# Performance work log

Hardware: AMD Instinct MI355X
Metric: run time of the kernel (lower is better)

## Reference

```python
import jax, jax.numpy as jnp
import numpy as np
import math

D_MODEL = 1024
NUM_HEADS = 16
D_KV = 64
INNER = NUM_HEADS * D_KV
NUM_BUCKETS = 32
MAX_DISTANCE = 128


def _relative_position_bucket(relative_position, num_buckets=NUM_BUCKETS, max_distance=MAX_DISTANCE):
    # bidirectional T5 bucketing
    n = -relative_position
    num_buckets = num_buckets // 2
    ret = (n < 0).astype(jnp.int32) * num_buckets
    n = jnp.abs(n)
    max_exact = num_buckets // 2
    is_small = n < max_exact
    n_safe = jnp.maximum(n, 1).astype(jnp.float32)  # avoid log(0); masked by is_small
    val_if_large = max_exact + (
        jnp.log(n_safe / max_exact) / math.log(max_distance / max_exact) * (num_buckets - max_exact)
    ).astype(jnp.int32)
    val_if_large = jnp.minimum(val_if_large, num_buckets - 1)
    return jnp.where(is_small, n, val_if_large) + ret


def _position_bias(rel_emb, q_len, k_len):
    ctx = jnp.arange(q_len)[:, None]
    mem = jnp.arange(k_len)[None, :]
    buckets = _relative_position_bucket(mem - ctx)          # [q, k]
    values = rel_emb[buckets]                               # [q, k, H]
    return jnp.transpose(values, (2, 0, 1))[None]           # [1, H, q, k]


def setup_inputs() -> dict:
    key = jax.random.key(0)
    ks = jax.random.split(key, 6)
    B, S = 2, 2048
    scale = 1.0 / math.sqrt(D_MODEL)
    return {
        "hidden_states": jax.random.normal(ks[0], (B, S, D_MODEL), dtype=jnp.float32),
        "mask": jnp.zeros((B, 1, 1, S), dtype=jnp.float32),
        "Wq": jax.random.normal(ks[1], (D_MODEL, INNER), dtype=jnp.float32) * scale,
        "Wk": jax.random.normal(ks[2], (D_MODEL, INNER), dtype=jnp.float32) * scale,
        "Wv": jax.random.normal(ks[3], (D_MODEL, INNER), dtype=jnp.float32) * scale,
        "Wo": jax.random.normal(ks[4], (INNER, D_MODEL), dtype=jnp.float32) * scale,
        "rel_emb": jax.random.normal(ks[5], (NUM_BUCKETS, NUM_HEADS), dtype=jnp.float32),
    }


def reference(hidden_states, mask, Wq, Wk, Wv, Wo, rel_emb):
    B, S, _ = hidden_states.shape
    def split_heads(x):
        return jnp.transpose(x.reshape(B, -1, NUM_HEADS, D_KV), (0, 2, 1, 3))  # [B,H,S,d]
    q = split_heads(hidden_states @ Wq)
    k = split_heads(hidden_states @ Wk)
    v = split_heads(hidden_states @ Wv)
    scores = jnp.einsum("bhqd,bhkd->bhqk", q, k)            # unscaled, T5-style
    position_bias = _position_bias(rel_emb, S, S)           # [1,H,S,S]
    scores = scores + position_bias + mask
    attn = jax.nn.softmax(scores, axis=-1)
    context = jnp.einsum("bhqk,bhkd->bhqd", attn, v)
    context = jnp.transpose(context, (0, 2, 1, 3)).reshape(B, S, INNER)
    output = context @ Wo
    return output, position_bias
```

## Files before the change

kernel.cpp:

```cpp
#include <hip/hip_runtime.h>
#include <cstdint>

#define AS1 __attribute__((address_space(1)))
#define AS3 __attribute__((address_space(3)))

typedef _Float16 half8 __attribute__((ext_vector_type(8)));
typedef _Float16 half4_t __attribute__((ext_vector_type(4)));
typedef float v4f __attribute__((ext_vector_type(4)));

__device__ __forceinline__ void async_ld16(const void* g, void* l) {
  __builtin_amdgcn_global_load_lds((const AS1 uint32_t*)g, (AS3 uint32_t*)l, 16, 0, 0);
}

__device__ __forceinline__ int t5_bucket(int delta) {
  int n = -delta;
  int ret = 0;
  if (n < 0) { ret = 16; n = -n; }
  if (n < 8) return n + ret;
  if (n >= 91) return 15 + ret;
  if ((n & (n - 1)) == 0) {
    int l = 31 - __clz(n);
    int v = 2 + 2 * l;
    return (v > 15 ? 15 : v) + ret;
  }
  int v = 8 + (int)(logf((float)n * 0.125f) * (8.0f / logf(16.0f)));
  return (v > 15 ? 15 : v) + ret;
}

__global__ void k_prep(const float* __restrict__ hs, const float* __restrict__ Wq,
                       const float* __restrict__ Wk, const float* __restrict__ Wv,
                       const float* __restrict__ Wo, _Float16* __restrict__ hsF,
                       _Float16* __restrict__ wqkvT, _Float16* __restrict__ woT) {
  const int tid = threadIdx.x;
  if (blockIdx.x < 4096) {
    int t = blockIdx.x * 256 + tid;
    float4 f = ((const float4*)hs)[t];
    half4_t h = {(_Float16)f.x, (_Float16)f.y, (_Float16)f.z, (_Float16)f.w};
    ((half4_t*)hsF)[t] = h;
    return;
  }
  __shared__ float tile[32][33];
  const int idx = blockIdx.x - 4096;
  const int z = idx >> 10, rem = idx & 1023;
  const float* src = (z == 0) ? Wq : (z == 1) ? Wk : (z == 2) ? Wv : Wo;
  _Float16* dst = (z < 3) ? (wqkvT + ((size_t)z << 20)) : woT;
  const int tx = tid & 31, ty = tid >> 5;
  const int bx = (rem & 31) * 32, by = (rem >> 5) * 32;
#pragma unroll
  for (int i = 0; i < 32; i += 8)
    tile[ty + i][tx] = src[(size_t)(by + ty + i) * 1024 + bx + tx];
  __syncthreads();
#pragma unroll
  for (int i = 0; i < 32; i += 8)
    dst[(size_t)(bx + ty + i) * 1024 + by + tx] = (_Float16)tile[tx][ty + i];
}

__global__ __launch_bounds__(256, 2) void k_gemm_qkv_bias(
    const _Float16* __restrict__ A, const _Float16* __restrict__ BT,
    _Float16* __restrict__ qkv, _Float16* __restrict__ vT,
    const float* __restrict__ rel, float* __restrict__ outb) {
  __shared__ __align__(16) _Float16 As[128 * 32];
  __shared__ __align__(16) _Float16 Bs[128 * 32];
  __shared__ float btab[256];
  const int tid = threadIdx.x;
  const int wave = tid >> 6, lane = tid & 63;
  const int l15 = lane & 15, quad = lane >> 4;
  const int m0 = blockIdx.y * 128, n0 = blockIdx.x * 128;
  const int wm = (wave >> 1) * 64, wn = (wave & 1) * 64;
  const int r0 = tid >> 2, c0 = (tid & 3) * 8;
  constexpr int K = 1024;

  const int bid = blockIdx.y * 24 + blockIdx.x;
  const bool do_bias = bid < 512;
  const int hB = bid >> 5;
  const int qoff = (bid & 31) * 64;
  float c_past = 0.f, c_fut = 0.f;
  if (do_bias) {
    btab[tid & 255] = rel[t5_bucket((tid & 255) - 128) * 16 + hB];
    c_past = rel[15 * 16 + hB];
    c_fut = rel[31 * 16 + hB];
  }

  v4f acc[4][4] = {};
  for (int k0 = 0; k0 < K; k0 += 32) {
    __syncthreads();
    async_ld16(A + (size_t)(m0 + r0) * K + k0 + c0, (char*)As + (size_t)(wave * 64) * 16);
    async_ld16(A + (size_t)(m0 + 64 + r0) * K + k0 + c0,
               (char*)As + (size_t)(256 + wave * 64) * 16);
    async_ld16(BT + (size_t)(n0 + r0) * K + k0 + c0, (char*)Bs + (size_t)(wave * 64) * 16);
    async_ld16(BT + (size_t)(n0 + 64 + r0) * K + k0 + c0,
               (char*)Bs + (size_t)(256 + wave * 64) * 16);
    __syncthreads();

    if (do_bias) {
      const int iter = k0 >> 5;
#pragma unroll
      for (int j = 0; j < 4; ++j) {
        int fi = iter * 1024 + j * 256 + tid;
        int qr = qoff + (fi >> 9);
        int kb = (fi & 511) * 4;
        float4 v;
        if (kb - qr >= 91) {
          v = make_float4(c_fut, c_fut, c_fut, c_fut);
        } else if (qr - kb - 3 >= 91) {
          v = make_float4(c_past, c_past, c_past, c_past);
        } else {
          v.x = btab[kb + 0 - qr + 128];
          v.y = btab[kb + 1 - qr + 128];
          v.z = btab[kb + 2 - qr + 128];
          v.w = btab[kb + 3 - qr + 128];
        }
        ((float4*)outb)[(size_t)bid * 32768 + fi] = v;
      }
    }

    half8 af[4], bf[4];
#pragma unroll
    for (int mt = 0; mt < 4; ++mt)
      af[mt] = *(const half8*)(As + (wm + mt * 16 + l15) * 32 + quad * 8);
#pragma unroll
    for (int nt = 0; nt < 4; ++nt)
      bf[nt] = *(const half8*)(Bs + (wn + nt * 16 + l15) * 32 + quad * 8);
#pragma unroll
    for (int mt = 0; mt < 4; ++mt)
#pragma unroll
      for (int nt = 0; nt < 4; ++nt)
        acc[mt][nt] = __builtin_amdgcn_mfma_f32_16x16x32_f16(af[mt], bf[nt], acc[mt][nt], 0, 0, 0);
  }
  if (n0 >= 2048) {
#pragma unroll
    for (int mt = 0; mt < 4; ++mt)
#pragma unroll
      for (int nt = 0; nt < 4; ++nt) {
        int col = n0 + wn + nt * 16 + l15 - 2048;
        int row0 = m0 + wm + mt * 16 + quad * 4;
        int bb = row0 >> 11, s0 = row0 & 2047;
        half4_t hv = {(_Float16)acc[mt][nt][0], (_Float16)acc[mt][nt][1],
                      (_Float16)acc[mt][nt][2], (_Float16)acc[mt][nt][3]};
        *(half4_t*)(vT + ((size_t)bb * 1024 + col) * 2048 + s0) = hv;
      }
    return;
  }
#pragma unroll
  for (int mt = 0; mt < 4; ++mt)
#pragma unroll
    for (int nt = 0; nt < 4; ++nt)
#pragma unroll
      for (int r = 0; r < 4; ++r)
        qkv[(size_t)(m0 + wm + mt * 16 + quad * 4 + r) * 3072 + n0 + wn + nt * 16 + l15] =
            (_Float16)acc[mt][nt][r];
}

__global__ __launch_bounds__(256, 2) void k_gemm_n64(const _Float16* __restrict__ A,
                                                     const _Float16* __restrict__ BT,
                                                     float* __restrict__ C, int K, int ldc) {
  __shared__ __align__(16) _Float16 As[128 * 32];
  __shared__ __align__(16) _Float16 Bs[64 * 32];
  const int tid = threadIdx.x;
  const int wave = tid >> 6, lane = tid & 63;
  const int l15 = lane & 15, quad = lane >> 4;
  const int m0 = blockIdx.y * 128, n0 = blockIdx.x * 64;
  const int wm = (wave >> 1) * 64, wn = (wave & 1) * 32;
  const int r0 = tid >> 2, c0 = (tid & 3) * 8;
  v4f acc[4][2] = {};
  for (int k0 = 0; k0 < K; k0 += 32) {
    __syncthreads();
    async_ld16(A + (size_t)(m0 + r0) * K + k0 + c0, (char*)As + (size_t)(wave * 64) * 16);
    async_ld16(A + (size_t)(m0 + 64 + r0) * K + k0 + c0,
               (char*)As + (size_t)(256 + wave * 64) * 16);
    async_ld16(BT + (size_t)(n0 + r0) * K + k0 + c0, (char*)Bs + (size_t)(wave * 64) * 16);
    __syncthreads();
    half8 af[4], bf[2];
#pragma unroll
    for (int mt = 0; mt < 4; ++mt)
      af[mt] = *(const half8*)(As + (wm + mt * 16 + l15) * 32 + quad * 8);
#pragma unroll
    for (int nt = 0; nt < 2; ++nt)
      bf[nt] = *(const half8*)(Bs + (wn + nt * 16 + l15) * 32 + quad * 8);
#pragma unroll
    for (int mt = 0; mt < 4; ++mt)
#pragma unroll
      for (int nt = 0; nt < 2; ++nt)
        acc[mt][nt] = __builtin_amdgcn_mfma_f32_16x16x32_f16(af[mt], bf[nt], acc[mt][nt], 0, 0, 0);
  }
#pragma unroll
  for (int mt = 0; mt < 4; ++mt)
#pragma unroll
    for (int nt = 0; nt < 2; ++nt)
#pragma unroll
      for (int r = 0; r < 4; ++r)
        C[(size_t)(m0 + wm + mt * 16 + quad * 4 + r) * ldc + n0 + wn + nt * 16 + l15] =
            acc[mt][nt][r];
}

__global__ __launch_bounds__(256, 2) void k_attn(const _Float16* __restrict__ qkv,
                                                 const _Float16* __restrict__ vT,
                                                 const float* __restrict__ mask,
                                                 const float* __restrict__ rel,
                                                 _Float16* __restrict__ ctx) {
  constexpr int S = 2048, LD = 3072;
  __shared__ __align__(16) _Float16 Ks[2][64 * 72];
  __shared__ __align__(16) _Float16 VT[2][64 * 72];
  __shared__ __align__(16) _Float16 Psh[128 * 72];
  __shared__ float btab[512];
  const int tid = threadIdx.x, wave = tid >> 6, lane = tid & 63;
  const int l15 = lane & 15, quad = lane >> 4;
  const int q0 = blockIdx.x * 128, h = blockIdx.y, b = blockIdx.z;

  for (int j = tid; j < 512; j += 256) btab[j] = rel[t5_bucket(j - 256) * 16 + h];
  const float c_past = rel[15 * 16 + h];
  const float c_fut = rel[31 * 16 + h];

  half8 bq[2][2];
#pragma unroll
  for (int qt = 0; qt < 2; ++qt) {
    const _Float16* qp = qkv + (size_t)(b * S + q0 + wave * 32 + qt * 16 + l15) * LD + h * 64;
    bq[qt][0] = *(const half8*)(qp + quad * 8);
    bq[qt][1] = *(const half8*)(qp + 32 + quad * 8);
  }
  v4f o[2][4] = {};
  float mrun[2] = {-INFINITY, -INFINITY};
  float lrun[2] = {0.f, 0.f};

  const int srow = tid >> 2, scol = (tid & 3) * 8;
  const _Float16* kg = qkv + (size_t)(b * S + srow) * LD + 1024 + h * 64 + scol;
  const _Float16* vg = vT + ((size_t)((b * 16 + h) * 64 + srow)) * S + scol;
  const float4* mkp = (const float4*)(mask + (size_t)b * S);

  {
    half8 kr0 = *(const half8*)(kg);
    half8 kr1 = *(const half8*)(kg + 32);
    half8 vr0 = *(const half8*)(vg);
    half8 vr1 = *(const half8*)(vg + 32);
    *(half8*)(&Ks[0][srow * 72 + scol]) = kr0;
    *(half8*)(&Ks[0][srow * 72 + scol + 32]) = kr1;
    *(half8*)(&VT[0][srow * 72 + scol]) = vr0;
    *(half8*)(&VT[0][srow * 72 + scol + 32]) = vr1;
  }
  float4 mk[4];
#pragma unroll
  for (int mt = 0; mt < 4; ++mt) mk[mt] = mkp[mt * 4 + quad];
  __syncthreads();

  for (int kv0 = 0; kv0 < S; kv0 += 64) {
    const int buf = (kv0 >> 6) & 1;
    const bool more = (kv0 + 64) < S;
    half8 kr0n, kr1n, vr0n, vr1n;
    float4 mkn[4];
    if (more) {
      kr0n = *(const half8*)(kg + (size_t)(kv0 + 64) * LD);
      kr1n = *(const half8*)(kg + (size_t)(kv0 + 64) * LD + 32);
      vr0n = *(const half8*)(vg + kv0 + 64);
      vr1n = *(const half8*)(vg + kv0 + 64 + 32);
#pragma unroll
      for (int mt = 0; mt < 4; ++mt) mkn[mt] = mkp[((kv0 + 64) >> 2) + mt * 4 + quad];
    }

    const _Float16* KsB = &Ks[buf][0];
    const _Float16* VTB = &VT[buf][0];
    v4f sc[2][4] = {};
#pragma unroll
    for (int kc = 0; kc < 2; ++kc)
#pragma unroll
      for (int mt = 0; mt < 4; ++mt) {
        half8 af = *(const half8*)(KsB + (mt * 16 + l15) * 72 + kc * 32 + quad * 8);
        sc[0][mt] = __builtin_amdgcn_mfma_f32_16x16x32_f16(af, bq[0][kc], sc[0][mt], 0, 0, 0);
        sc[1][mt] = __builtin_amdgcn_mfma_f32_16x16x32_f16(af, bq[1][kc], sc[1][mt], 0, 0, 0);
      }

    const int diff = kv0 - q0;
    const bool mixed = (diff >= -153) && (diff <= 217);
    const float cf = (diff >= 218) ? c_fut : c_past;
    v4f cm[4];
#pragma unroll
    for (int mt = 0; mt < 4; ++mt) {
      cm[mt][0] = mk[mt].x; cm[mt][1] = mk[mt].y; cm[mt][2] = mk[mt].z; cm[mt][3] = mk[mt].w;
      if (!mixed) {
        cm[mt][0] += cf; cm[mt][1] += cf; cm[mt][2] += cf; cm[mt][3] += cf;
      }
    }
    if (mixed) {
#pragma unroll
      for (int qt = 0; qt < 2; ++qt) {
        const int qq = q0 + wave * 32 + qt * 16 + l15;
#pragma unroll
        for (int mt = 0; mt < 4; ++mt) {
          int base = kv0 + mt * 16 + quad * 4 - qq + 256;
#pragma unroll
          for (int r = 0; r < 4; ++r) sc[qt][mt][r] += btab[base + r] + cm[mt][r];
        }
      }
    } else {
#pragma unroll
      for (int qt = 0; qt < 2; ++qt)
#pragma unroll
        for (int mt = 0; mt < 4; ++mt)
#pragma unroll
          for (int r = 0; r < 4; ++r) sc[qt][mt][r] += cm[mt][r];
    }

#pragma unroll
    for (int qt = 0; qt < 2; ++qt) {
      v4f m4 = sc[qt][0];
#pragma unroll
      for (int r = 0; r < 4; ++r) {
        m4[r] = fmaxf(m4[r], sc[qt][1][r]);
        m4[r] = fmaxf(m4[r], sc[qt][2][r]);
        m4[r] = fmaxf(m4[r], sc[qt][3][r]);
      }
      float mx = fmaxf(fmaxf(m4[0], m4[1]), fmaxf(m4[2], m4[3]));
      mx = fmaxf(mx, __shfl_xor(mx, 16, 64));
      mx = fmaxf(mx, __shfl_xor(mx, 32, 64));
      float mnew = fmaxf(mrun[qt], mx);
      float alpha = __expf(mrun[qt] - mnew);
      mrun[qt] = mnew;
      v4f s4 = {};
#pragma unroll
      for (int mt = 0; mt < 4; ++mt)
#pragma unroll
        for (int r = 0; r < 4; ++r) {
          float p = __expf(sc[qt][mt][r] - mnew);
          sc[qt][mt][r] = p;
          s4[r] += p;
        }
      float rs = (s4[0] + s4[1]) + (s4[2] + s4[3]);
      rs += __shfl_xor(rs, 16, 64);
      rs += __shfl_xor(rs, 32, 64);
      lrun[qt] = lrun[qt] * alpha + rs;
#pragma unroll
      for (int dt = 0; dt < 4; ++dt)
#pragma unroll
        for (int r = 0; r < 4; ++r) o[qt][dt][r] *= alpha;
      const int prow = wave * 32 + qt * 16 + l15;
#pragma unroll
      for (int mt = 0; mt < 4; ++mt) {
        half4_t ph = {(_Float16)sc[qt][mt][0], (_Float16)sc[qt][mt][1],
                      (_Float16)sc[qt][mt][2], (_Float16)sc[qt][mt][3]};
        *(half4_t*)(Psh + prow * 72 + mt * 16 + quad * 4) = ph;
      }
    }

#pragma unroll
    for (int kc = 0; kc < 2; ++kc) {
      half8 bp0 = *(const half8*)(Psh + (wave * 32 + l15) * 72 + kc * 32 + quad * 8);
      half8 bp1 = *(const half8*)(Psh + (wave * 32 + 16 + l15) * 72 + kc * 32 + quad * 8);
#pragma unroll
      for (int dt = 0; dt < 4; ++dt) {
        half8 av = *(const half8*)(VTB + (dt * 16 + l15) * 72 + kc * 32 + quad * 8);
        o[0][dt] = __builtin_amdgcn_mfma_f32_16x16x32_f16(av, bp0, o[0][dt], 0, 0, 0);
        o[1][dt] = __builtin_amdgcn_mfma_f32_16x16x32_f16(av, bp1, o[1][dt], 0, 0, 0);
      }
    }

    if (more) {
      _Float16* Kn = &Ks[buf ^ 1][0];
      _Float16* Vn = &VT[buf ^ 1][0];
      *(half8*)(Kn + srow * 72 + scol) = kr0n;
      *(half8*)(Kn + srow * 72 + scol + 32) = kr1n;
      *(half8*)(Vn + srow * 72 + scol) = vr0n;
      *(half8*)(Vn + srow * 72 + scol + 32) = vr1n;
      __syncthreads();
#pragma unroll
      for (int mt = 0; mt < 4; ++mt) mk[mt] = mkn[mt];
    }
  }
#pragma unroll
  for (int qt = 0; qt < 2; ++qt) {
    float inv = 1.0f / lrun[qt];
    const size_t token = (size_t)(b * S + q0 + wave * 32 + qt * 16 + l15);
#pragma unroll
    for (int dt = 0; dt < 4; ++dt) {
      half4_t hv = {(_Float16)(o[qt][dt][0] * inv), (_Float16)(o[qt][dt][1] * inv),
                    (_Float16)(o[qt][dt][2] * inv), (_Float16)(o[qt][dt][3] * inv)};
      *(half4_t*)(ctx + token * 1024 + h * 64 + dt * 16 + quad * 4) = hv;
    }
  }
}

extern "C" void kernel_launch(void* const* d_in, const int* in_sizes, int n_in,
                              void* d_out, int out_size, void* d_ws, size_t ws_size,
                              hipStream_t stream) {
  const float* hs = (const float*)d_in[0];
  const float* mask = (const float*)d_in[1];
  const float* Wq = (const float*)d_in[2];
  const float* Wk = (const float*)d_in[3];
  const float* Wv = (const float*)d_in[4];
  const float* Wo = (const float*)d_in[5];
  const float* rel = (const float*)d_in[6];
  float* out = (float*)d_out;

  char* ws = (char*)d_ws;
  _Float16* hsF = (_Float16*)(ws);
  _Float16* wqkvT = (_Float16*)(ws + (8u << 20));
  _Float16* woT = (_Float16*)(ws + (14u << 20));
  _Float16* qkv = (_Float16*)(ws + (16u << 20));
  _Float16* ctx = (_Float16*)(ws + (40u << 20));
  _Float16* vT = (_Float16*)(ws + (48u << 20));

  k_prep<<<8192, 256, 0, stream>>>(hs, Wq, Wk, Wv, Wo, hsF, wqkvT, woT);

  k_gemm_qkv_bias<<<dim3(24, 32), 256, 0, stream>>>(hsF, wqkvT, qkv, vT, rel,
                                                    out + 4194304);
  k_attn<<<dim3(16, 16, 2), 256, 0, stream>>>(qkv, vT, mask, rel, ctx);
  k_gemm_n64<<<dim3(16, 32), 256, 0, stream>>>(ctx, woT, out, 1024, 1024);
}
```

Baseline: 427.4 us.

## Split position-bias output writes between QKV GEMM and attention kernels; skip redundant rescale

```diff
diff --git a/kernel.cpp b/kernel.cpp
--- a/kernel.cpp
+++ b/kernel.cpp
@@ -95,10 +95,12 @@
     if (do_bias) {
       const int iter = k0 >> 5;
 #pragma unroll
-      for (int j = 0; j < 4; ++j) {
-        int fi = iter * 1024 + j * 256 + tid;
-        int qr = qoff + (fi >> 9);
-        int kb = (fi & 511) * 4;
+      for (int j = 0; j < 2; ++j) {
+        int fi = iter * 512 + j * 256 + tid;
+        int qr = qoff + (fi >> 8);
+        int c = fi & 255;
+        int k4 = ((c >> 4) << 5) + (c & 15);
+        int kb = k4 << 2;
         float4 v;
         if (kb - qr >= 91) {
           v = make_float4(c_fut, c_fut, c_fut, c_fut);
@@ -110,7 +112,7 @@
           v.z = btab[kb + 2 - qr + 128];
           v.w = btab[kb + 3 - qr + 128];
         }
-        ((float4*)outb)[(size_t)bid * 32768 + fi] = v;
+        ((float4*)outb)[((size_t)hB * 2048 + qr) * 512 + k4] = v;
       }
     }
 
@@ -197,7 +199,8 @@
                                                  const _Float16* __restrict__ vT,
                                                  const float* __restrict__ mask,
                                                  const float* __restrict__ rel,
-                                                 _Float16* __restrict__ ctx) {
+                                                 _Float16* __restrict__ ctx,
+                                                 float* __restrict__ outb) {
   constexpr int S = 2048, LD = 3072;
   __shared__ __align__(16) _Float16 Ks[2][64 * 72];
   __shared__ __align__(16) _Float16 VT[2][64 * 72];
@@ -226,6 +229,9 @@
   const _Float16* kg = qkv + (size_t)(b * S + srow) * LD + 1024 + h * 64 + scol;
   const _Float16* vg = vT + ((size_t)((b * 16 + h) * 64 + srow)) * S + scol;
   const float4* mkp = (const float4*)(mask + (size_t)b * S);
+
+  const int qrow0 = q0 + b * 64;
+  float4* const bias_base = (float4*)outb + ((size_t)h * 2048 + qrow0) * 512;
 
   {
     half8 kr0 = *(const half8*)(kg);
@@ -256,6 +262,46 @@
       for (int mt = 0; mt < 4; ++mt) mkn[mt] = mkp[((kv0 + 64) >> 2) + mt * 4 + quad];
     }
 
+    if (kv0 & 64) {
+      const int diffw = kv0 - qrow0;
+      float4* dst = bias_base + (kv0 >> 2);
+      if (diffw >= 154) {
+        const float4 v = make_float4(c_fut, c_fut, c_fut, c_fut);
+#pragma unroll
+        for (int j = 0; j < 4; ++j) {
+          int fi = j * 256 + tid;
+          dst[(size_t)(fi >> 4) * 512 + (fi & 15)] = v;
+        }
+      } else if (diffw <= -154) {
+        const float4 v = make_float4(c_past, c_past, c_past, c_past);
+#pragma unroll
+        for (int j = 0; j < 4; ++j) {
+          int fi = j * 256 + tid;
+          dst[(size_t)(fi >> 4) * 512 + (fi & 15)] = v;
+        }
+      } else {
+#pragma unroll
+        for (int j = 0; j < 4; ++j) {
+          int fi = j * 256 + tid;
+          int row = fi >> 4, c4 = fi & 15;
+          int q = qrow0 + row, k = kv0 + c4 * 4;
+          float4 v;
+          if (k - q >= 91) {
+            v = make_float4(c_fut, c_fut, c_fut, c_fut);
+          } else if (q - k - 3 >= 91) {
+            v = make_float4(c_past, c_past, c_past, c_past);
+          } else {
+            int bi = k - q + 256;
+            v.x = btab[bi + 0];
+            v.y = btab[bi + 1];
+            v.z = btab[bi + 2];
+            v.w = btab[bi + 3];
+          }
+          dst[(size_t)row * 512 + c4] = v;
+        }
+      }
+    }
+
     const _Float16* KsB = &Ks[buf][0];
     const _Float16* VTB = &VT[buf][0];
     v4f sc[2][4] = {};
@@ -311,26 +357,30 @@
       float mx = fmaxf(fmaxf(m4[0], m4[1]), fmaxf(m4[2], m4[3]));
       mx = fmaxf(mx, __shfl_xor(mx, 16, 64));
       mx = fmaxf(mx, __shfl_xor(mx, 32, 64));
-      float mnew = fmaxf(mrun[qt], mx);
-      float alpha = __expf(mrun[qt] - mnew);
-      mrun[qt] = mnew;
+      if (!__all(mx <= mrun[qt])) {
+        float mnew = fmaxf(mrun[qt], mx);
+        float alpha = __expf(mrun[qt] - mnew);
+        mrun[qt] = mnew;
+        lrun[qt] *= alpha;
+#pragma unroll
+        for (int dt = 0; dt < 4; ++dt)
+#pragma unroll
+          for (int r = 0; r < 4; ++r) o[qt][dt][r] *= alpha;
+      }
+      const float mcur = mrun[qt];
       v4f s4 = {};
 #pragma unroll
       for (int mt = 0; mt < 4; ++mt)
 #pragma unroll
         for (int r = 0; r < 4; ++r) {
-          float p = __expf(sc[qt][mt][r] - mnew);
+          float p = __expf(sc[qt][mt][r] - mcur);
           sc[qt][mt][r] = p;
           s4[r] += p;
         }
       float rs = (s4[0] + s4[1]) + (s4[2] + s4[3]);
       rs += __shfl_xor(rs, 16, 64);
       rs += __shfl_xor(rs, 32, 64);
-      lrun[qt] = lrun[qt] * alpha + rs;
-#pragma unroll
-      for (int dt = 0; dt < 4; ++dt)
-#pragma unroll
-        for (int r = 0; r < 4; ++r) o[qt][dt][r] *= alpha;
+      lrun[qt] += rs;
       const int prow = wave * 32 + qt * 16 + l15;
 #pragma unroll
       for (int mt = 0; mt < 4; ++mt) {
@@ -401,6 +451,6 @@
 
   k_gemm_qkv_bias<<<dim3(24, 32), 256, 0, stream>>>(hsF, wqkvT, qkv, vT, rel,
                                                     out + 4194304);
-  k_attn<<<dim3(16, 16, 2), 256, 0, stream>>>(qkv, vT, mask, rel, ctx);
+  k_attn<<<dim3(16, 16, 2), 256, 0, stream>>>(qkv, vT, mask, rel, ctx, out + 4194304);
   k_gemm_n64<<<dim3(16, 32), 256, 0, stream>>>(ctx, woT, out, 1024, 1024);
 }
```

Result: no change. 420.7 us (-1.6%).
